# Kernel optimization log

Hardware: AMD Instinct MI355X
Metric: run time of the kernel (lower is better)

Reference implementation:

```python
import jax, jax.numpy as jnp
import numpy as np

N, E, D, L = 100000, 1600000, 32, 5


def setup_inputs() -> dict:
    key = jax.random.key(0)
    ks = jax.random.split(key, 8)
    s = 1.0 / np.sqrt(D)
    return {
        "x": jax.random.normal(ks[0], (N, D), dtype=jnp.float32),
        "edge_attr": jax.random.normal(ks[1], (E, D), dtype=jnp.float32),
        "edge_index": jax.random.randint(ks[2], (2, E), 0, N, dtype=jnp.int64),
        "W1": jax.random.normal(ks[3], (L, D, D), dtype=jnp.float32) * s,
        "b1": jnp.zeros((L, D), dtype=jnp.float32),
        "W2": jax.random.normal(ks[4], (L, D, D), dtype=jnp.float32) * s,
        "b2": jnp.zeros((L, D), dtype=jnp.float32),
        "eps": jnp.zeros((L,), dtype=jnp.float32),  # train_eps=True, init 0
    }


def reference(x, edge_attr, edge_index, W1, b1, W2, b2, eps):
    # GINEConv x num_layers: aggr_i = sum_j relu(x_j + e_ij); out = MLP((1+eps)*x_i + aggr_i)
    src = edge_index[0]  # j (message source)
    dst = edge_index[1]  # i (message target)
    n = x.shape[0]
    for l in range(W1.shape[0]):
        msg = jax.nn.relu(x[src] + edge_attr)                  # [E, D]
        aggr = jax.ops.segment_sum(msg, dst, num_segments=n)    # [N, D]
        h = (1.0 + eps[l]) * x + aggr
        h = jax.nn.relu(h @ W1[l] + b1[l]) @ W2[l] + b2[l]      # inner MLP
        x = jax.nn.relu(h)                                      # outer relu in forward
    return x
```

## Files before the change

kernel.cpp:

```cpp
#include <hip/hip_runtime.h>

#define D 32
#define NPB 64
#define SRC_BITS 25
#define SRC_MASK ((1 << SRC_BITS) - 1)
#define SCAN_CHUNK 1024

__device__ __forceinline__ float relu_f(float v) { return v > 0.f ? v : 0.f; }

__device__ __forceinline__ unsigned bf16_rne(float f) {
    unsigned u = __float_as_uint(f);
    return (u + 0x7FFFu + ((u >> 16) & 1u)) >> 16;
}

__global__ void __launch_bounds__(256) hist_kernel(
    const int* __restrict__ dst, int* __restrict__ deg, int E)
{
    int e = blockIdx.x * 256 + threadIdx.x;
    if (e < E) atomicAdd(&deg[dst[e]], 1);
}

__global__ void __launch_bounds__(256) scan_partial_kernel(
    const int* __restrict__ deg, int* __restrict__ part, int N)
{
    __shared__ int s[256];
    int t = threadIdx.x;
    int base = blockIdx.x * SCAN_CHUNK + t * 4;
    int sum = 0;
    #pragma unroll
    for (int i = 0; i < 4; ++i) { int idx = base + i; if (idx < N) sum += deg[idx]; }
    s[t] = sum;
    __syncthreads();
    for (int off = 128; off > 0; off >>= 1) {
        if (t < off) s[t] += s[t + off];
        __syncthreads();
    }
    if (t == 0) part[blockIdx.x] = s[0];
}

__global__ void scan_part_exclusive_kernel(int* part, int nb)
{
    if (threadIdx.x == 0 && blockIdx.x == 0) {
        int run = 0;
        for (int i = 0; i < nb; ++i) { int v = part[i]; part[i] = run; run += v; }
    }
}

__global__ void __launch_bounds__(256) scan_final_kernel(
    int* __restrict__ rowdeg, const int* __restrict__ part, int N)
{
    __shared__ int s[256];
    int t = threadIdx.x;
    int base = blockIdx.x * SCAN_CHUNK + t * 4;
    int d0 = 0, d1 = 0, d2 = 0, d3 = 0;
    if (base + 0 < N) d0 = rowdeg[base + 0];
    if (base + 1 < N) d1 = rowdeg[base + 1];
    if (base + 2 < N) d2 = rowdeg[base + 2];
    if (base + 3 < N) d3 = rowdeg[base + 3];
    int tsum = d0 + d1 + d2 + d3;
    s[t] = tsum;
    __syncthreads();
    for (int off = 1; off < 256; off <<= 1) {
        int a = (t >= off) ? s[t - off] : 0;
        __syncthreads();
        s[t] += a;
        __syncthreads();
    }
    int excl = s[t] - tsum + part[blockIdx.x];
    if (base + 0 < N) rowdeg[base + 0] = excl;
    if (base + 1 < N) rowdeg[base + 1] = excl + d0;
    if (base + 2 < N) rowdeg[base + 2] = excl + d0 + d1;
    if (base + 3 < N) rowdeg[base + 3] = excl + d0 + d1 + d2;
}

__global__ void __launch_bounds__(256) place_full_kernel(
    const int* __restrict__ src, const int* __restrict__ dst,
    const float* __restrict__ ea, int* __restrict__ row,
    int* __restrict__ srcpk, unsigned* __restrict__ eah, int E)
{
    int i = blockIdx.x * 256 + threadIdx.x;
    if (i >= E * 8) return;
    int e = i >> 3, q = i & 7;
    int pos = 0;
    if (q == 0) {
        int d = dst[e];
        pos = atomicAdd(&row[d], 1);
        srcpk[pos] = src[e] | ((d & (NPB - 1)) << SRC_BITS);
    }
    pos = __shfl(pos, 0, 8);
    float4 v = reinterpret_cast<const float4*>(ea)[(size_t)e * 8 + q];
    uint2 w;
    w.x = bf16_rne(v.x) | (bf16_rne(v.y) << 16);
    w.y = bf16_rne(v.z) | (bf16_rne(v.w) << 16);
    reinterpret_cast<uint2*>(eah)[(size_t)pos * 8 + q] = w;
}

__global__ void __launch_bounds__(256) place_csr_kernel(
    const int* __restrict__ src, const int* __restrict__ dst,
    int* __restrict__ row, int* __restrict__ srcperm,
    int* __restrict__ eperm, int E)
{
    int e = blockIdx.x * 256 + threadIdx.x;
    if (e < E) {
        int pos = atomicAdd(&row[dst[e]], 1);
        srcperm[pos] = src[e];
        eperm[pos] = e;
    }
}

__global__ void __launch_bounds__(256) gine_fused3_kernel(
    const float* __restrict__ x, const unsigned* __restrict__ eah,
    const int* __restrict__ srcpk, const int* __restrict__ row,
    const float* __restrict__ W1, const float* __restrict__ b1,
    const float* __restrict__ W2, const float* __restrict__ b2,
    const float* __restrict__ eps, int l, float* __restrict__ out, int N)
{
    __shared__ float aggr[NPB][D];
    __shared__ float W1s[D * D], W2s[D * D];
    __shared__ float b1s[D], b2s[D];
    __shared__ float ys[8][D];

    int t = threadIdx.x;
    for (int i = t; i < D * D; i += 256) { W1s[i] = W1[i]; W2s[i] = W2[i]; }
    if (t < D) { b1s[t] = b1[t]; b2s[t] = b2[t]; }
    for (int i = t; i < NPB * D; i += 256) ((float*)aggr)[i] = 0.f;

    int g8 = t >> 3;
    int q  = t & 7;
    int n0 = blockIdx.x * NPB;
    int nlast = min(n0 + NPB - 1, N - 1);
    int estart = n0 ? row[n0 - 1] : 0;
    int eend   = row[nlast];
    __syncthreads();

    int EB = eend - estart;
    int chunk = (EB + 31) >> 5;
    int a = estart + g8 * chunk;
    int b = min(a + chunk, eend);

    float4 acc = make_float4(0.f, 0.f, 0.f, 0.f);
    int cur = -1;
    int k = a;
    while (k + 8 <= b) {
        int pv = srcpk[k + q];
        #pragma unroll
        for (int i = 0; i < 8; ++i) {
            int p  = __shfl(pv, i, 8);
            int s  = p & SRC_MASK;
            int ld = (p >> SRC_BITS) & (NPB - 1);
            uint2 w = *reinterpret_cast<const uint2*>(eah + (size_t)(k + i) * 8 + q);
            float4 xv = *reinterpret_cast<const float4*>(x + (size_t)s * D + q * 4);
            if (ld != cur) {
                if (cur >= 0) {
                    atomicAdd(&aggr[cur][q * 4 + 0], acc.x);
                    atomicAdd(&aggr[cur][q * 4 + 1], acc.y);
                    atomicAdd(&aggr[cur][q * 4 + 2], acc.z);
                    atomicAdd(&aggr[cur][q * 4 + 3], acc.w);
                }
                cur = ld;
                acc = make_float4(0.f, 0.f, 0.f, 0.f);
            }
            acc.x += relu_f(xv.x + __uint_as_float(w.x << 16));
            acc.y += relu_f(xv.y + __uint_as_float(w.x & 0xFFFF0000u));
            acc.z += relu_f(xv.z + __uint_as_float(w.y << 16));
            acc.w += relu_f(xv.w + __uint_as_float(w.y & 0xFFFF0000u));
        }
        k += 8;
    }
    while (k < b) {
        int p  = srcpk[k];
        int s  = p & SRC_MASK;
        int ld = (p >> SRC_BITS) & (NPB - 1);
        uint2 w = *reinterpret_cast<const uint2*>(eah + (size_t)k * 8 + q);
        float4 xv = *reinterpret_cast<const float4*>(x + (size_t)s * D + q * 4);
        if (ld != cur) {
            if (cur >= 0) {
                atomicAdd(&aggr[cur][q * 4 + 0], acc.x);
                atomicAdd(&aggr[cur][q * 4 + 1], acc.y);
                atomicAdd(&aggr[cur][q * 4 + 2], acc.z);
                atomicAdd(&aggr[cur][q * 4 + 3], acc.w);
            }
            cur = ld;
            acc = make_float4(0.f, 0.f, 0.f, 0.f);
        }
        acc.x += relu_f(xv.x + __uint_as_float(w.x << 16));
        acc.y += relu_f(xv.y + __uint_as_float(w.x & 0xFFFF0000u));
        acc.z += relu_f(xv.z + __uint_as_float(w.y << 16));
        acc.w += relu_f(xv.w + __uint_as_float(w.y & 0xFFFF0000u));
        ++k;
    }
    if (cur >= 0) {
        atomicAdd(&aggr[cur][q * 4 + 0], acc.x);
        atomicAdd(&aggr[cur][q * 4 + 1], acc.y);
        atomicAdd(&aggr[cur][q * 4 + 2], acc.z);
        atomicAdd(&aggr[cur][q * 4 + 3], acc.w);
    }
    __syncthreads();

    int hw = t >> 5, j = t & 31;
    float ep1 = 1.0f + eps[l];
    for (int r = 0; r < 8; ++r) {
        int ln = hw * 8 + r;
        int n = n0 + ln;
        if (n >= N) break;
        float h = ep1 * x[(size_t)n * D + j] + aggr[ln][j];
        aggr[ln][j] = h;
        float a1 = b1s[j];
        #pragma unroll
        for (int kk = 0; kk < D; ++kk)
            a1 = fmaf(aggr[ln][kk], W1s[kk * D + j], a1);
        float y = relu_f(a1);
        ys[hw][j] = y;
        float a2 = b2s[j];
        #pragma unroll
        for (int kk = 0; kk < D; ++kk)
            a2 = fmaf(ys[hw][kk], W2s[kk * D + j], a2);
        out[(size_t)n * D + j] = relu_f(a2);
    }
}

__global__ void __launch_bounds__(256) gine_fused_kernel(
    const float* __restrict__ x, const float* __restrict__ ea,
    const int* __restrict__ srcperm, const int* __restrict__ eperm,
    const int* __restrict__ row,
    const float* __restrict__ W1, const float* __restrict__ b1,
    const float* __restrict__ W2, const float* __restrict__ b2,
    const float* __restrict__ eps, int l, float* __restrict__ out, int N)
{
    __shared__ float W1s[D * D], W2s[D * D], b1s[D], b2s[D];
    int t = threadIdx.x;
    for (int i = t; i < D * D; i += 256) { W1s[i] = W1[i]; W2s[i] = W2[i]; }
    if (t < D) { b1s[t] = b1[t]; b2s[t] = b2[t]; }
    __syncthreads();

    int g = t >> 5, j = t & 31;
    int node = blockIdx.x * 8 + g;
    if (node >= N) return;
    int start = node ? row[node - 1] : 0;
    int end = row[node];

    float acc = 0.f;
    for (int k = start; k < end; ++k) {
        int s0 = srcperm[k];
        float e0 = ea[(size_t)eperm[k] * D + j];
        acc += relu_f(x[(size_t)s0 * D + j] + e0);
    }
    float h = (1.0f + eps[l]) * x[(size_t)node * D + j] + acc;
    float a1 = b1s[j];
    #pragma unroll
    for (int kk = 0; kk < D; ++kk)
        a1 = fmaf(__shfl(h, kk, 32), W1s[kk * D + j], a1);
    float y = relu_f(a1);
    float a2 = b2s[j];
    #pragma unroll
    for (int kk = 0; kk < D; ++kk)
        a2 = fmaf(__shfl(y, kk, 32), W2s[kk * D + j], a2);
    out[(size_t)node * D + j] = relu_f(a2);
}

__global__ void __launch_bounds__(256) gine_scatter_kernel(
    const float* __restrict__ x, const float* __restrict__ ea,
    const int* __restrict__ src, const int* __restrict__ dst,
    float* __restrict__ aggr, int E)
{
    int i = blockIdx.x * blockDim.x + threadIdx.x;
    if (i >= E * 8) return;
    int e = i >> 3, q = i & 7;
    float4 a = reinterpret_cast<const float4*>(ea)[(size_t)e * 8 + q];
    int s = src[e], d = dst[e];
    float4 xv = reinterpret_cast<const float4*>(x)[(size_t)s * 8 + q];
    float* base = aggr + (size_t)d * D + (size_t)q * 4;
    __hip_atomic_fetch_add(base + 0, relu_f(xv.x + a.x), __ATOMIC_RELAXED, __HIP_MEMORY_SCOPE_AGENT);
    __hip_atomic_fetch_add(base + 1, relu_f(xv.y + a.y), __ATOMIC_RELAXED, __HIP_MEMORY_SCOPE_AGENT);
    __hip_atomic_fetch_add(base + 2, relu_f(xv.z + a.z), __ATOMIC_RELAXED, __HIP_MEMORY_SCOPE_AGENT);
    __hip_atomic_fetch_add(base + 3, relu_f(xv.w + a.w), __ATOMIC_RELAXED, __HIP_MEMORY_SCOPE_AGENT);
}

__global__ void __launch_bounds__(256) gine_node_kernel(
    const float* __restrict__ x, const float* __restrict__ aggr,
    const float* __restrict__ W1, const float* __restrict__ b1,
    const float* __restrict__ W2, const float* __restrict__ b2,
    const float* __restrict__ eps, int l, float* __restrict__ out, int N)
{
    __shared__ float W1s[D * D], W2s[D * D], b1s[D], b2s[D];
    __shared__ float hs[8][D], y1s[8][D];
    int t = threadIdx.x;
    for (int i = t; i < D * D; i += 256) { W1s[i] = W1[i]; W2s[i] = W2[i]; }
    if (t < D) { b1s[t] = b1[t]; b2s[t] = b2[t]; }
    float ep1 = 1.0f + eps[l];
    int local = t >> 5, j = t & 31;
    int node = blockIdx.x * 8 + local;
    __syncthreads();
    if (node < N)
        hs[local][j] = ep1 * x[(size_t)node * D + j] + aggr[(size_t)node * D + j];
    __syncthreads();
    if (node < N) {
        float acc = b1s[j];
        #pragma unroll
        for (int k = 0; k < D; ++k) acc = fmaf(hs[local][k], W1s[k * D + j], acc);
        y1s[local][j] = relu_f(acc);
    }
    __syncthreads();
    if (node < N) {
        float acc = b2s[j];
        #pragma unroll
        for (int k = 0; k < D; ++k) acc = fmaf(y1s[local][k], W2s[k * D + j], acc);
        out[(size_t)node * D + j] = relu_f(acc);
    }
}

extern "C" void kernel_launch(void* const* d_in, const int* in_sizes, int n_in,
                              void* d_out, int out_size, void* d_ws, size_t ws_size,
                              hipStream_t stream) {
    const float* x_in = (const float*)d_in[0];
    const float* ea   = (const float*)d_in[1];
    const int*   ei   = (const int*)d_in[2];
    const float* W1   = (const float*)d_in[3];
    const float* b1   = (const float*)d_in[4];
    const float* W2   = (const float*)d_in[5];
    const float* b2   = (const float*)d_in[6];
    const float* eps  = (const float*)d_in[7];

    int N = in_sizes[0] / D;
    int E = in_sizes[1] / D;
    int L = in_sizes[3] / (D * D);

    const int* src = ei;
    const int* dst = ei + E;

    float* out = (float*)d_out;
    char*  ws  = (char*)d_ws;

    size_t off = 0;
    auto take = [&](size_t bytes) -> size_t {
        size_t p = off; off = (off + bytes + 255) & ~(size_t)255; return p;
    };
    size_t o_bufA    = take((size_t)N * D * sizeof(float));
    size_t o_row     = take((size_t)(N + 8) * sizeof(int));
    size_t o_part    = take(1024 * sizeof(int));
    size_t o_srcpk   = take((size_t)E * sizeof(int));
    size_t base_need = off;
    size_t o_eperm   = base_need;
    size_t need_csr  = base_need + (((size_t)E * sizeof(int) + 255) & ~(size_t)255);
    size_t o_eah     = base_need;
    size_t need_full = base_need + (size_t)E * D * sizeof(unsigned short);

    float* bufA  = (float*)(ws + o_bufA);
    int*   row   = (int*)(ws + o_row);
    int*   part  = (int*)(ws + o_part);
    int*   srcpk = (int*)(ws + o_srcpk);

    int path = (ws_size >= need_full) ? 2 : (ws_size >= need_csr ? 1 : 0);

    if (path == 0) {
        float* aggr = bufA + (size_t)N * D;
        const float* cur = x_in;
        for (int l = 0; l < L; ++l) {
            float* nxt = (((L - 1 - l) & 1) == 0) ? out : bufA;
            hipMemsetAsync(aggr, 0, (size_t)N * D * sizeof(float), stream);
            gine_scatter_kernel<<<(E * 8 + 255) / 256, 256, 0, stream>>>(cur, ea, src, dst, aggr, E);
            gine_node_kernel<<<(N + 7) / 8, 256, 0, stream>>>(
                cur, aggr, W1 + (size_t)l * D * D, b1 + (size_t)l * D,
                W2 + (size_t)l * D * D, b2 + (size_t)l * D, eps, l, nxt, N);
            cur = nxt;
        }
        return;
    }

    int*      eperm = (int*)(ws + o_eperm);
    unsigned* eah   = (unsigned*)(ws + o_eah);

    int nb = (N + SCAN_CHUNK - 1) / SCAN_CHUNK;
    hipMemsetAsync(row, 0, (size_t)N * sizeof(int), stream);
    hist_kernel<<<(E + 255) / 256, 256, 0, stream>>>(dst, row, E);
    scan_partial_kernel<<<nb, 256, 0, stream>>>(row, part, N);
    scan_part_exclusive_kernel<<<1, 64, 0, stream>>>(part, nb);
    scan_final_kernel<<<nb, 256, 0, stream>>>(row, part, N);
    if (path == 2) {
        place_full_kernel<<<(E * 8 + 255) / 256, 256, 0, stream>>>(
            src, dst, ea, row, srcpk, eah, E);
    } else {
        place_csr_kernel<<<(E + 255) / 256, 256, 0, stream>>>(
            src, dst, row, srcpk, eperm, E);
    }

    const float* cur = x_in;
    for (int l = 0; l < L; ++l) {
        float* nxt = (((L - 1 - l) & 1) == 0) ? out : bufA;
        if (path == 2) {
            gine_fused3_kernel<<<(N + NPB - 1) / NPB, 256, 0, stream>>>(
                cur, eah, srcpk, row,
                W1 + (size_t)l * D * D, b1 + (size_t)l * D,
                W2 + (size_t)l * D * D, b2 + (size_t)l * D, eps, l, nxt, N);
        } else {
            gine_fused_kernel<<<(N + 7) / 8, 256, 0, stream>>>(
                cur, ea, srcpk, eperm, row,
                W1 + (size_t)l * D * D, b1 + (size_t)l * D,
                W2 + (size_t)l * D * D, b2 + (size_t)l * D, eps, l, nxt, N);
        }
        cur = nxt;
    }
}
```

Measured before the change: 535.5 us.

## Split edge placement into index pass plus gather-convert, batch loads in aggregation loop

The old fused placement kernel, which scattered bf16 edge features, is replaced by two kernels. The first places source/packed indices and an edge permutation into CSR order. The second gathers fp32 edge_attr through that permutation and writes the bf16 copy contiguously, so the writes coalesce instead of scattering. Separately, the aggregation inner loop now issues all eight edge and x loads before any accumulation, which raises memory-level parallelism at the cost of extra registers. The workspace now always reserves eperm alongside eah, and the CSR fallback masks the packed bits.

```diff
diff --git a/kernel.cpp b/kernel.cpp
--- a/kernel.cpp
+++ b/kernel.cpp
@@ -73,42 +73,36 @@
     if (base + 3 < N) rowdeg[base + 3] = excl + d0 + d1 + d2;
 }
 
-__global__ void __launch_bounds__(256) place_full_kernel(
+__global__ void __launch_bounds__(256) place_idx_kernel(
     const int* __restrict__ src, const int* __restrict__ dst,
-    const float* __restrict__ ea, int* __restrict__ row,
-    int* __restrict__ srcpk, unsigned* __restrict__ eah, int E)
+    int* __restrict__ row, int* __restrict__ srcpk,
+    int* __restrict__ eperm, int E)
+{
+    int e = blockIdx.x * 256 + threadIdx.x;
+    if (e < E) {
+        int d = dst[e];
+        int pos = atomicAdd(&row[d], 1);
+        srcpk[pos] = src[e] | ((d & (NPB - 1)) << SRC_BITS);
+        eperm[pos] = e;
+    }
+}
+
+__global__ void __launch_bounds__(256) gather_convert_kernel(
+    const float* __restrict__ ea, const int* __restrict__ eperm,
+    unsigned* __restrict__ eah, int E)
 {
     int i = blockIdx.x * 256 + threadIdx.x;
     if (i >= E * 8) return;
-    int e = i >> 3, q = i & 7;
-    int pos = 0;
-    if (q == 0) {
-        int d = dst[e];
-        pos = atomicAdd(&row[d], 1);
-        srcpk[pos] = src[e] | ((d & (NPB - 1)) << SRC_BITS);
-    }
-    pos = __shfl(pos, 0, 8);
+    int p = i >> 3, q = i & 7;
+    int e = eperm[p];
     float4 v = reinterpret_cast<const float4*>(ea)[(size_t)e * 8 + q];
     uint2 w;
     w.x = bf16_rne(v.x) | (bf16_rne(v.y) << 16);
     w.y = bf16_rne(v.z) | (bf16_rne(v.w) << 16);
-    reinterpret_cast<uint2*>(eah)[(size_t)pos * 8 + q] = w;
-}
-
-__global__ void __launch_bounds__(256) place_csr_kernel(
-    const int* __restrict__ src, const int* __restrict__ dst,
-    int* __restrict__ row, int* __restrict__ srcperm,
-    int* __restrict__ eperm, int E)
-{
-    int e = blockIdx.x * 256 + threadIdx.x;
-    if (e < E) {
-        int pos = atomicAdd(&row[dst[e]], 1);
-        srcperm[pos] = src[e];
-        eperm[pos] = e;
-    }
-}
-
-__global__ void __launch_bounds__(256) gine_fused3_kernel(
+    reinterpret_cast<uint2*>(eah)[(size_t)p * 8 + q] = w;
+}
+
+__global__ void __launch_bounds__(256) gine_fused4_kernel(
     const float* __restrict__ x, const unsigned* __restrict__ eah,
     const int* __restrict__ srcpk, const int* __restrict__ row,
     const float* __restrict__ W1, const float* __restrict__ b1,
@@ -143,13 +137,20 @@
     int k = a;
     while (k + 8 <= b) {
         int pv = srcpk[k + q];
+        uint2  w[8];
+        float4 xv[8];
+        int    pp[8];
         #pragma unroll
         for (int i = 0; i < 8; ++i) {
             int p  = __shfl(pv, i, 8);
+            pp[i] = p;
             int s  = p & SRC_MASK;
-            int ld = (p >> SRC_BITS) & (NPB - 1);
-            uint2 w = *reinterpret_cast<const uint2*>(eah + (size_t)(k + i) * 8 + q);
-            float4 xv = *reinterpret_cast<const float4*>(x + (size_t)s * D + q * 4);
+            w[i]  = *reinterpret_cast<const uint2*>(eah + (size_t)(k + i) * 8 + q);
+            xv[i] = *reinterpret_cast<const float4*>(x + (size_t)s * D + q * 4);
+        }
+        #pragma unroll
+        for (int i = 0; i < 8; ++i) {
+            int ld = (pp[i] >> SRC_BITS) & (NPB - 1);
             if (ld != cur) {
                 if (cur >= 0) {
                     atomicAdd(&aggr[cur][q * 4 + 0], acc.x);
@@ -160,10 +161,10 @@
                 cur = ld;
                 acc = make_float4(0.f, 0.f, 0.f, 0.f);
             }
-            acc.x += relu_f(xv.x + __uint_as_float(w.x << 16));
-            acc.y += relu_f(xv.y + __uint_as_float(w.x & 0xFFFF0000u));
-            acc.z += relu_f(xv.z + __uint_as_float(w.y << 16));
-            acc.w += relu_f(xv.w + __uint_as_float(w.y & 0xFFFF0000u));
+            acc.x += relu_f(xv[i].x + __uint_as_float(w[i].x << 16));
+            acc.y += relu_f(xv[i].y + __uint_as_float(w[i].x & 0xFFFF0000u));
+            acc.z += relu_f(xv[i].z + __uint_as_float(w[i].y << 16));
+            acc.w += relu_f(xv[i].w + __uint_as_float(w[i].y & 0xFFFF0000u));
         }
         k += 8;
     }
@@ -241,7 +242,7 @@
 
     float acc = 0.f;
     for (int k = start; k < end; ++k) {
-        int s0 = srcperm[k];
+        int s0 = srcperm[k] & SRC_MASK;
         float e0 = ea[(size_t)eperm[k] * D + j];
         acc += relu_f(x[(size_t)s0 * D + j] + e0);
     }
@@ -339,16 +340,16 @@
     size_t o_row     = take((size_t)(N + 8) * sizeof(int));
     size_t o_part    = take(1024 * sizeof(int));
     size_t o_srcpk   = take((size_t)E * sizeof(int));
-    size_t base_need = off;
-    size_t o_eperm   = base_need;
-    size_t need_csr  = base_need + (((size_t)E * sizeof(int) + 255) & ~(size_t)255);
-    size_t o_eah     = base_need;
-    size_t need_full = base_need + (size_t)E * D * sizeof(unsigned short);
+    size_t o_eperm   = take((size_t)E * sizeof(int));
+    size_t need_csr  = off;
+    size_t o_eah     = take((size_t)E * D * sizeof(unsigned short));
+    size_t need_full = off;
 
     float* bufA  = (float*)(ws + o_bufA);
     int*   row   = (int*)(ws + o_row);
     int*   part  = (int*)(ws + o_part);
     int*   srcpk = (int*)(ws + o_srcpk);
+    int*   eperm = (int*)(ws + o_eperm);
 
     int path = (ws_size >= need_full) ? 2 : (ws_size >= need_csr ? 1 : 0);
 
@@ -367,8 +368,7 @@
         return;
     }
 
-    int*      eperm = (int*)(ws + o_eperm);
-    unsigned* eah   = (unsigned*)(ws + o_eah);
+    unsigned* eah = (unsigned*)(ws + o_eah);
 
     int nb = (N + SCAN_CHUNK - 1) / SCAN_CHUNK;
     hipMemsetAsync(row, 0, (size_t)N * sizeof(int), stream);
@@ -376,19 +376,18 @@
     scan_partial_kernel<<<nb, 256, 0, stream>>>(row, part, N);
     scan_part_exclusive_kernel<<<1, 64, 0, stream>>>(part, nb);
     scan_final_kernel<<<nb, 256, 0, stream>>>(row, part, N);
+    place_idx_kernel<<<(E + 255) / 256, 256, 0, stream>>>(
+        src, dst, row, srcpk, eperm, E);
     if (path == 2) {
-        place_full_kernel<<<(E * 8 + 255) / 256, 256, 0, stream>>>(
-            src, dst, ea, row, srcpk, eah, E);
-    } else {
-        place_csr_kernel<<<(E + 255) / 256, 256, 0, stream>>>(
-            src, dst, row, srcpk, eperm, E);
+        gather_convert_kernel<<<(E * 8 + 255) / 256, 256, 0, stream>>>(
+            ea, eperm, eah, E);
     }
 
     const float* cur = x_in;
     for (int l = 0; l < L; ++l) {
         float* nxt = (((L - 1 - l) & 1) == 0) ? out : bufA;
         if (path == 2) {
-            gine_fused3_kernel<<<(N + NPB - 1) / NPB, 256, 0, stream>>>(
+            gine_fused4_kernel<<<(N + NPB - 1) / NPB, 256, 0, stream>>>(
                 cur, eah, srcpk, row,
                 W1 + (size_t)l * D * D, b1 + (size_t)l * D,
                 W2 + (size_t)l * D * D, b2 + (size_t)l * D, eps, l, nxt, N);
```

Result: slower. 588.9 us (+10.0%).

## Pipeline edge gathers into LDS with async global_load_lds triple buffering

Applied to the files above, without the earlier changes.

The fused GINE layer kernel now stages each block's packed source indices into shared memory and uses per-wave async global-to-LDS loads to prefetch tiles of bf16 edge attributes and gathered x rows. Three slots are kept in flight, with explicit vmcnt waits. The aim is to hide gather latency behind the relu-accumulate work. It adds a large LDS footprint (weights plus about 45KB of staging), which may lower occupancy, and relies on hand-counted waitcnt values. It also separates the eperm and eah workspace regions and packs the local dst into the CSR fallback path.

```diff
diff --git a/kernel.cpp b/kernel.cpp
--- a/kernel.cpp
+++ b/kernel.cpp
@@ -5,12 +5,21 @@
 #define SRC_BITS 25
 #define SRC_MASK ((1 << SRC_BITS) - 1)
 #define SCAN_CHUNK 1024
+#define PKCAP 2048
+#define TILE 16
+#define NSLOT 3
 
 __device__ __forceinline__ float relu_f(float v) { return v > 0.f ? v : 0.f; }
 
 __device__ __forceinline__ unsigned bf16_rne(float f) {
     unsigned u = __float_as_uint(f);
     return (u + 0x7FFFu + ((u >> 16) & 1u)) >> 16;
+}
+
+__device__ __forceinline__ void async16(const void* g, void* l) {
+    __builtin_amdgcn_global_load_lds(
+        (const __attribute__((address_space(1))) void*)g,
+        (__attribute__((address_space(3))) void*)l, 16, 0, 0);
 }
 
 __global__ void __launch_bounds__(256) hist_kernel(
@@ -103,83 +112,62 @@
     int e = blockIdx.x * 256 + threadIdx.x;
     if (e < E) {
         int pos = atomicAdd(&row[dst[e]], 1);
-        srcperm[pos] = src[e];
+        srcperm[pos] = src[e] | ((dst[e] & (NPB - 1)) << SRC_BITS);
         eperm[pos] = e;
     }
 }
 
-__global__ void __launch_bounds__(256) gine_fused3_kernel(
-    const float* __restrict__ x, const unsigned* __restrict__ eah,
+__global__ void __launch_bounds__(256) gine_fused5_kernel(
+    const float* __restrict__ x, const uint2* __restrict__ eah,
     const int* __restrict__ srcpk, const int* __restrict__ row,
     const float* __restrict__ W1, const float* __restrict__ b1,
     const float* __restrict__ W2, const float* __restrict__ b2,
     const float* __restrict__ eps, int l, float* __restrict__ out, int N)
 {
+    __shared__ float W1s[D * D], W2s[D * D], b1s[D], b2s[D];
     __shared__ float aggr[NPB][D];
-    __shared__ float W1s[D * D], W2s[D * D];
-    __shared__ float b1s[D], b2s[D];
     __shared__ float ys[8][D];
+    __shared__ int   pkL[PKCAP];
+    __shared__ __align__(16) char stg[4][NSLOT][3072];
 
     int t = threadIdx.x;
-    for (int i = t; i < D * D; i += 256) { W1s[i] = W1[i]; W2s[i] = W2[i]; }
-    if (t < D) { b1s[t] = b1[t]; b2s[t] = b2[t]; }
-    for (int i = t; i < NPB * D; i += 256) ((float*)aggr)[i] = 0.f;
-
-    int g8 = t >> 3;
-    int q  = t & 7;
     int n0 = blockIdx.x * NPB;
     int nlast = min(n0 + NPB - 1, N - 1);
     int estart = n0 ? row[n0 - 1] : 0;
     int eend   = row[nlast];
-    __syncthreads();
-
     int EB = eend - estart;
-    int chunk = (EB + 31) >> 5;
-    int a = estart + g8 * chunk;
-    int b = min(a + chunk, eend);
+    int staged = min(EB, PKCAP);
+
+    for (int i = t; i < D * D; i += 256) { W1s[i] = W1[i]; W2s[i] = W2[i]; }
+    if (t < D) { b1s[t] = b1[t]; b2s[t] = b2[t]; }
+    for (int i = t; i < NPB * D; i += 256) ((float*)aggr)[i] = 0.f;
+    for (int i = t; i < staged; i += 256) pkL[i] = srcpk[estart + i];
+    __syncthreads();
+
+    int wv = t >> 6;
+    int ln = t & 63;
+    int g  = (t >> 3) & 7;
+    int q  = t & 7;
+
+    int cw = (staged + 3) >> 2;
+    int a0 = min(wv * cw, staged);
+    int b0 = min(a0 + cw, staged);
+    int nt = (b0 - a0) >> 4;
 
     float4 acc = make_float4(0.f, 0.f, 0.f, 0.f);
     int cur = -1;
-    int k = a;
-    while (k + 8 <= b) {
-        int pv = srcpk[k + q];
-        #pragma unroll
-        for (int i = 0; i < 8; ++i) {
-            int p  = __shfl(pv, i, 8);
-            int s  = p & SRC_MASK;
-            int ld = (p >> SRC_BITS) & (NPB - 1);
-            uint2 w = *reinterpret_cast<const uint2*>(eah + (size_t)(k + i) * 8 + q);
-            float4 xv = *reinterpret_cast<const float4*>(x + (size_t)s * D + q * 4);
-            if (ld != cur) {
-                if (cur >= 0) {
-                    atomicAdd(&aggr[cur][q * 4 + 0], acc.x);
-                    atomicAdd(&aggr[cur][q * 4 + 1], acc.y);
-                    atomicAdd(&aggr[cur][q * 4 + 2], acc.z);
-                    atomicAdd(&aggr[cur][q * 4 + 3], acc.w);
-                }
-                cur = ld;
-                acc = make_float4(0.f, 0.f, 0.f, 0.f);
-            }
-            acc.x += relu_f(xv.x + __uint_as_float(w.x << 16));
-            acc.y += relu_f(xv.y + __uint_as_float(w.x & 0xFFFF0000u));
-            acc.z += relu_f(xv.z + __uint_as_float(w.y << 16));
-            acc.w += relu_f(xv.w + __uint_as_float(w.y & 0xFFFF0000u));
-        }
-        k += 8;
-    }
-    while (k < b) {
-        int p  = srcpk[k];
-        int s  = p & SRC_MASK;
-        int ld = (p >> SRC_BITS) & (NPB - 1);
-        uint2 w = *reinterpret_cast<const uint2*>(eah + (size_t)k * 8 + q);
-        float4 xv = *reinterpret_cast<const float4*>(x + (size_t)s * D + q * 4);
+
+    auto flush = [&]() {
+        if (cur >= 0) {
+            atomicAdd(&aggr[cur][q * 4 + 0], acc.x);
+            atomicAdd(&aggr[cur][q * 4 + 1], acc.y);
+            atomicAdd(&aggr[cur][q * 4 + 2], acc.z);
+            atomicAdd(&aggr[cur][q * 4 + 3], acc.w);
+        }
+    };
+    auto edge = [&](int ld, uint2 w, float4 xv) {
         if (ld != cur) {
-            if (cur >= 0) {
-                atomicAdd(&aggr[cur][q * 4 + 0], acc.x);
-                atomicAdd(&aggr[cur][q * 4 + 1], acc.y);
-                atomicAdd(&aggr[cur][q * 4 + 2], acc.z);
-                atomicAdd(&aggr[cur][q * 4 + 3], acc.w);
-            }
+            flush();
             cur = ld;
             acc = make_float4(0.f, 0.f, 0.f, 0.f);
         }
@@ -187,28 +175,76 @@
         acc.y += relu_f(xv.y + __uint_as_float(w.x & 0xFFFF0000u));
         acc.z += relu_f(xv.z + __uint_as_float(w.y << 16));
         acc.w += relu_f(xv.w + __uint_as_float(w.y & 0xFFFF0000u));
-        ++k;
-    }
-    if (cur >= 0) {
-        atomicAdd(&aggr[cur][q * 4 + 0], acc.x);
-        atomicAdd(&aggr[cur][q * 4 + 1], acc.y);
-        atomicAdd(&aggr[cur][q * 4 + 2], acc.z);
-        atomicAdd(&aggr[cur][q * 4 + 3], acc.w);
-    }
+    };
+
+    auto stage = [&](int tt) {
+        int kk = estart + a0 + tt * TILE;
+        char* sl = stg[wv][tt % NSLOT];
+        async16((const char*)eah + (size_t)kk * 64 + ln * 16, sl);
+        #pragma unroll
+        for (int c = 0; c < 2; ++c) {
+            int pk = pkL[a0 + tt * TILE + c * 8 + (ln >> 3)];
+            async16((const char*)x + (size_t)(pk & SRC_MASK) * 128 + (ln & 7) * 16,
+                    sl + 1024 + c * 1024);
+        }
+    };
+    auto compute = [&](int tt) {
+        int kk0 = a0 + tt * TILE;
+        const char* sl = stg[wv][tt % NSLOT];
+        #pragma unroll
+        for (int c = 0; c < 2; ++c) {
+            int pk = pkL[kk0 + c * 8 + g];
+            uint2  w  = *reinterpret_cast<const uint2*>(sl + (c * 8 + g) * 64 + q * 8);
+            float4 xv = *reinterpret_cast<const float4*>(sl + 1024 + c * 1024 + g * 128 + q * 16);
+            edge((pk >> SRC_BITS) & (NPB - 1), w, xv);
+        }
+    };
+
+    if (nt > 0) stage(0);
+    if (nt > 1) stage(1);
+    for (int tt = 0; tt < nt; ++tt) {
+        if (tt + 2 < nt) {
+            stage(tt + 2);
+            asm volatile("s_waitcnt vmcnt(6)" ::: "memory");
+        } else if (tt + 1 < nt) {
+            asm volatile("s_waitcnt vmcnt(3)" ::: "memory");
+        } else {
+            asm volatile("s_waitcnt vmcnt(0)" ::: "memory");
+        }
+        compute(tt);
+    }
+
+    auto tail = [&](int lo, int hi) {
+        for (int e = lo + g; e < hi; e += 8) {
+            int pk = srcpk[estart + e];
+            uint2 w = eah[(size_t)(estart + e) * 8 + q];
+            float4 xv = *reinterpret_cast<const float4*>(x + (size_t)(pk & SRC_MASK) * D + q * 4);
+            edge((pk >> SRC_BITS) & (NPB - 1), w, xv);
+        }
+    };
+    tail(a0 + nt * TILE, b0);
+    if (EB > staged) {
+        int ovn = EB - staged;
+        int c2 = (ovn + 3) >> 2;
+        int o0 = staged + min(wv * c2, ovn);
+        int o1 = min(o0 + c2, EB);
+        tail(o0, o1);
+    }
+    flush();
     __syncthreads();
 
     int hw = t >> 5, j = t & 31;
     float ep1 = 1.0f + eps[l];
     for (int r = 0; r < 8; ++r) {
-        int ln = hw * 8 + r;
-        int n = n0 + ln;
+        int ln2 = hw * 8 + r;
+        int n = n0 + ln2;
         if (n >= N) break;
-        float h = ep1 * x[(size_t)n * D + j] + aggr[ln][j];
-        aggr[ln][j] = h;
+        float h = ep1 * x[(size_t)n * D + j] + aggr[ln2][j];
+        aggr[ln2][j] = h;
         float a1 = b1s[j];
         #pragma unroll
         for (int kk = 0; kk < D; ++kk)
-            a1 = fmaf(aggr[ln][kk], W1s[kk * D + j], a1);
+            a1 = fmaf(aggr[ln2][kk], W1s[kk * D + j], a1);
         float y = relu_f(a1);
         ys[hw][j] = y;
         float a2 = b2s[j];
@@ -241,7 +277,7 @@
 
     float acc = 0.f;
     for (int k = start; k < end; ++k) {
-        int s0 = srcperm[k];
+        int s0 = srcperm[k] & SRC_MASK;
         float e0 = ea[(size_t)eperm[k] * D + j];
         acc += relu_f(x[(size_t)s0 * D + j] + e0);
     }
@@ -339,16 +375,16 @@
     size_t o_row     = take((size_t)(N + 8) * sizeof(int));
     size_t o_part    = take(1024 * sizeof(int));
     size_t o_srcpk   = take((size_t)E * sizeof(int));
-    size_t base_need = off;
-    size_t o_eperm   = base_need;
-    size_t need_csr  = base_need + (((size_t)E * sizeof(int) + 255) & ~(size_t)255);
-    size_t o_eah     = base_need;
-    size_t need_full = base_need + (size_t)E * D * sizeof(unsigned short);
+    size_t o_eperm   = take((size_t)E * sizeof(int));
+    size_t need_csr  = off;
+    size_t o_eah     = take((size_t)E * D * sizeof(unsigned short));
+    size_t need_full = off;
 
     float* bufA  = (float*)(ws + o_bufA);
     int*   row   = (int*)(ws + o_row);
     int*   part  = (int*)(ws + o_part);
     int*   srcpk = (int*)(ws + o_srcpk);
+    int*   eperm = (int*)(ws + o_eperm);
 
     int path = (ws_size >= need_full) ? 2 : (ws_size >= need_csr ? 1 : 0);
 
@@ -367,8 +403,7 @@
         return;
     }
 
-    int*      eperm = (int*)(ws + o_eperm);
-    unsigned* eah   = (unsigned*)(ws + o_eah);
+    unsigned* eah = (unsigned*)(ws + o_eah);
 
     int nb = (N + SCAN_CHUNK - 1) / SCAN_CHUNK;
     hipMemsetAsync(row, 0, (size_t)N * sizeof(int), stream);
@@ -388,8 +423,8 @@
     for (int l = 0; l < L; ++l) {
         float* nxt = (((L - 1 - l) & 1) == 0) ? out : bufA;
         if (path == 2) {
-            gine_fused3_kernel<<<(N + NPB - 1) / NPB, 256, 0, stream>>>(
-                cur, eah, srcpk, row,
+            gine_fused5_kernel<<<(N + NPB - 1) / NPB, 256, 0, stream>>>(
+                cur, (const uint2*)eah, srcpk, row,
                 W1 + (size_t)l * D * D, b1 + (size_t)l * D,
                 W2 + (size_t)l * D * D, b2 + (size_t)l * D, eps, l, nxt, N);
         } else {
```

New measurement: 1.175 ms. +119.4%, slower.
